# Optimization experiments

Hardware: AMD Instinct MI355X
Metric: run time of the kernel (lower is better)

Reference implementation:

```python
import jax, jax.numpy as jnp
import numpy as np

D_MODEL = 512
NUM_HEADS = 8
HEAD_DIM = D_MODEL // NUM_HEADS  # 64
B, L = 8, 1024


def setup_inputs() -> dict:
    key = jax.random.key(0)
    ks = jax.random.split(key, 6)
    scale = 1.0 / np.sqrt(D_MODEL)
    return {
        "x": jax.random.normal(ks[0], (B, L, D_MODEL), dtype=jnp.float32),
        "mask": jax.random.normal(ks[1], (L, L), dtype=jnp.float32),
        "Wqkv": jax.random.normal(ks[2], (D_MODEL, 3 * D_MODEL), dtype=jnp.float32) * scale,
        "bqkv": jax.random.normal(ks[3], (3 * D_MODEL,), dtype=jnp.float32) * 0.01,
        "Wo": jax.random.normal(ks[4], (D_MODEL, D_MODEL), dtype=jnp.float32) * scale,
        "bo": jax.random.normal(ks[5], (D_MODEL,), dtype=jnp.float32) * 0.01,
    }


def reference(x, mask, Wqkv, bqkv, Wo, bo):
    b, l, _ = x.shape
    qkv = x @ Wqkv + bqkv                                   # [B, L, 3*D]
    # Faithful to torch: reshape to [B, L, H, 3*head_dim] then chunk last dim.
    qkv = qkv.reshape(b, l, NUM_HEADS, 3 * HEAD_DIM)
    qkv = jnp.transpose(qkv, (0, 2, 1, 3))                  # [B, H, L, 3*hd]
    q, k, v = jnp.split(qkv, 3, axis=-1)                    # each [B, H, L, hd]
    scaled = jnp.einsum("bhqd,bhkd->bhqk", q, k) / np.sqrt(HEAD_DIM)
    scaled = scaled + mask                                  # mask broadcasts over [B, H]
    attn = jax.nn.softmax(scaled, axis=-1)
    out = jnp.einsum("bhqk,bhkd->bhqd", attn, v)            # [B, H, L, hd]
    out = jnp.transpose(out, (0, 2, 1, 3)).reshape(b, l, D_MODEL)
    return out @ Wo + bo
```

## Files before the change

kernel.cpp:

```cpp
#include <hip/hip_runtime.h>
#include <hip/hip_bf16.h>
#include <stdint.h>

#define B_ 8
#define L_ 1024
#define DM 512
#define H_ 8
#define HD 64
#define N3 1536
#define M_T (B_*L_)
#define LOG2E 1.44269504f

typedef __attribute__((ext_vector_type(8))) short short8;
typedef __attribute__((ext_vector_type(4))) float f32x4;
typedef __attribute__((ext_vector_type(4))) float float4_t;
typedef __attribute__((ext_vector_type(4))) unsigned short ushort4_t;
typedef __attribute__((ext_vector_type(2))) unsigned int u32x2;

#define MFMA16(a,b,c) __builtin_amdgcn_mfma_f32_16x16x32_bf16((a),(b),(c),0,0,0)

__device__ __forceinline__ short f2bf(float f){
  union { float f; unsigned u; } v; v.f = f;
  unsigned r = v.u + 0x7fffu + ((v.u >> 16) & 1u);
  return (short)(r >> 16);
}

__device__ __forceinline__ short f2bf_fast(float f){
  __hip_bfloat16 h = __float2bfloat16(f);
  short s; __builtin_memcpy(&s, &h, 2); return s;
}

__global__ __launch_bounds__(256) void k_cvt(const float* __restrict__ x,
                                             short* __restrict__ xb, int n8){
  int i = blockIdx.x*256 + threadIdx.x;
  if (i >= n8) return;
  const float4_t* p = (const float4_t*)x + (size_t)i*2;
  float4_t a = p[0], b = p[1];
  short8 o;
  o[0]=f2bf(a[0]); o[1]=f2bf(a[1]); o[2]=f2bf(a[2]); o[3]=f2bf(a[3]);
  o[4]=f2bf(b[0]); o[5]=f2bf(b[1]); o[6]=f2bf(b[2]); o[7]=f2bf(b[3]);
  *((short8*)xb + i) = o;
}

__global__ __launch_bounds__(256) void k_tr2(const float* __restrict__ W0, short* __restrict__ WT0,
                                             const float* __restrict__ W1, short* __restrict__ WT1){
  __shared__ float t[64][65];
  const float* W; short* WT; int N, n0;
  if (blockIdx.x < 24){ W = W0; WT = WT0; N = N3; n0 = blockIdx.x*64; }
  else                { W = W1; WT = WT1; N = DM; n0 = (blockIdx.x-24)*64; }
  int k0 = blockIdx.y*64;
  int tid = threadIdx.x;
  int r = tid >> 4, c4 = (tid & 15) * 4;
  #pragma unroll
  for (int it=0; it<4; ++it){
    int rr = r + it*16;
    float4_t v = *(const float4_t*)(W + (size_t)(k0+rr)*N + n0 + c4);
    t[rr][c4+0]=v[0]; t[rr][c4+1]=v[1]; t[rr][c4+2]=v[2]; t[rr][c4+3]=v[3];
  }
  __syncthreads();
  #pragma unroll
  for (int it=0; it<4; ++it){
    int n = r + it*16;
    ushort4_t o;
    o[0]=(unsigned short)f2bf(t[c4+0][n]);
    o[1]=(unsigned short)f2bf(t[c4+1][n]);
    o[2]=(unsigned short)f2bf(t[c4+2][n]);
    o[3]=(unsigned short)f2bf(t[c4+3][n]);
    *(ushort4_t*)(WT + (size_t)(n0+n)*DM + k0 + c4) = o;
  }
}

__global__ __launch_bounds__(256) void k_maskp(const float* __restrict__ mask,
                                               float* __restrict__ maskP){
  int gid = blockIdx.x*256 + threadIdx.x;
  int nf  = gid & 3;
  int lane= (gid>>2) & 63;
  int kvt = (gid>>8) & 15;
  int qg  = gid>>12;
  int li = lane & 15, lg = lane >> 4;
  int row = qg*16 + li;
  int col = kvt*64 + nf*16 + lg*4;
  float4_t m = *(const float4_t*)(mask + (size_t)row*1024 + col);
  float4_t o;
  #pragma unroll
  for (int j=0;j<4;++j) o[j] = fmaf(m[j], LOG2E, -17.3123405f);
  ((float4_t*)maskP)[gid] = o;
}

__global__ __launch_bounds__(256) void k_gemm_qkv(
    const short* __restrict__ A, const short* __restrict__ Bt,
    const float* __restrict__ bias,
    short* __restrict__ Qo, short* __restrict__ Ko, short* __restrict__ VTo)
{
  __shared__ __align__(16) short As[2][128*40];
  __shared__ __align__(16) short Bs[2][128*40];
  const int m0 = blockIdx.x*128, n0 = blockIdx.y*128;
  const int tid = threadIdx.x;
  const int w = tid>>6, lane = tid&63, li = lane&15, lg = lane>>4;
  const int wr = (w>>1)*64, wc = (w&1)*64;

  int row[2], seg[2];
  #pragma unroll
  for (int c=0;c<2;++c){ int s = tid + c*256; row[c]=s>>2; seg[c]=s&3; }

  short8 ga[2], gb[2];
  #pragma unroll
  for (int c=0;c<2;++c){
    ga[c] = *(const short8*)(A  + (size_t)(m0+row[c])*DM + seg[c]*8);
    gb[c] = *(const short8*)(Bt + (size_t)(n0+row[c])*DM + seg[c]*8);
  }

  const f32x4 fz = {0.f,0.f,0.f,0.f};
  f32x4 acc[4][4];
  #pragma unroll
  for (int i=0;i<4;++i)
    #pragma unroll
    for (int j=0;j<4;++j) acc[i][j] = fz;

  for (int kt=0; kt<16; ++kt){
    short* as = As[kt&1]; short* bs = Bs[kt&1];
    #pragma unroll
    for (int c=0;c<2;++c){
      *(short8*)&as[row[c]*40 + seg[c]*8] = ga[c];
      *(short8*)&bs[row[c]*40 + seg[c]*8] = gb[c];
    }
    __syncthreads();
    if (kt < 15){
      int k0 = (kt+1)*32;
      #pragma unroll
      for (int c=0;c<2;++c){
        ga[c] = *(const short8*)(A  + (size_t)(m0+row[c])*DM + k0 + seg[c]*8);
        gb[c] = *(const short8*)(Bt + (size_t)(n0+row[c])*DM + k0 + seg[c]*8);
      }
    }
    short8 bfr[4];
    #pragma unroll
    for (int nf=0;nf<4;++nf)
      bfr[nf] = *(const short8*)&bs[(wc + nf*16 + li)*40 + lg*8];
    __builtin_amdgcn_s_setprio(1);
    #pragma unroll
    for (int mf=0;mf<4;++mf){
      short8 af = *(const short8*)&as[(wr + mf*16 + li)*40 + lg*8];
      #pragma unroll
      for (int nf=0;nf<4;++nf)
        acc[mf][nf] = MFMA16(af, bfr[nf], acc[mf][nf]);
    }
    __builtin_amdgcn_s_setprio(0);
    __syncthreads();
  }

  #pragma unroll
  for (int nf=0;nf<4;++nf){
    int n = n0 + wc + nf*16 + li;
    float bv = bias[n];
    unsigned h  = (unsigned)n / 192u;
    unsigned wn = (unsigned)n % 192u;
    unsigned typ = wn >> 6, d = wn & 63u;
    #pragma unroll
    for (int mf=0;mf<4;++mf){
      #pragma unroll
      for (int j=0;j<4;++j){
        int m  = m0 + wr + mf*16 + lg*4 + j;
        int b  = m >> 10, lp = m & 1023;
        size_t bh = (size_t)(b*8 + (int)h);
        float vf = acc[mf][nf][j] + bv;
        if (typ == 0)      Qo [(bh<<16) + ((size_t)lp<<6)  + d]  = f2bf_fast(vf * 0.18033688f);
        else if (typ == 1) Ko [(bh<<16) + ((size_t)lp<<6)  + d]  = f2bf_fast(vf);
        else               VTo[(bh<<16) + ((size_t)d<<10)  + lp] = f2bf_fast(vf);
      }
    }
  }
}

__global__ __launch_bounds__(256, 2) void k_attn(
    const short* __restrict__ Q, const short* __restrict__ Kb,
    const short* __restrict__ VT, const float* __restrict__ maskP,
    short* __restrict__ O2)
{
  __shared__ __align__(16) short Ks[2][64*72];
  __shared__ __align__(16) short Vs[2][64*72];
  __shared__ __align__(16) short Ps[4][32*72];
  const int bh = blockIdx.y;
  const int q0 = blockIdx.x*128;
  const int tid = threadIdx.x, w = tid>>6, lane = tid&63, li = lane&15, lg = lane>>4;
  const int qw = q0 + w*32;

  const short* Qp = Q  + ((size_t)bh<<16);
  const short* Kp = Kb + ((size_t)bh<<16);
  const short* Vp = VT + ((size_t)bh<<16);

  short8 qf[2][2];
  #pragma unroll
  for (int mb=0;mb<2;++mb)
    #pragma unroll
    for (int t=0;t<2;++t)
      qf[mb][t] = *(const short8*)(Qp + ((size_t)(qw+mb*16+li)<<6) + t*32 + lg*8);

  short8 ones8;
  #pragma unroll
  for (int e=0;e<8;++e) ones8[e] = (short)0x3f80;

  const f32x4 fz = {0.f,0.f,0.f,0.f};
  f32x4 o[2][4], osum[2];
  #pragma unroll
  for (int mb=0;mb<2;++mb){
    osum[mb] = fz;
    #pragma unroll
    for (int df=0;df<4;++df) o[mb][df] = fz;
  }

  int srow[2], sseg[2];
  #pragma unroll
  for (int c=0;c<2;++c){ int f = tid + c*256; srow[c]=f>>3; sseg[c]=(f&7)*8; }

  short8 gk[2], gv[2];
  #pragma unroll
  for (int c=0;c<2;++c){
    gk[c] = *(const short8*)(Kp + ((size_t)srow[c]<<6)  + sseg[c]);
    gv[c] = *(const short8*)(Vp + ((size_t)srow[c]<<10) + sseg[c]);
  }
  #pragma unroll
  for (int c=0;c<2;++c){
    *(short8*)&Ks[0][srow[c]*72 + sseg[c]] = gk[c];
    *(short8*)&Vs[0][srow[c]*72 + sseg[c]] = gv[c];
  }
  #pragma unroll
  for (int c=0;c<2;++c){
    gk[c] = *(const short8*)(Kp + ((size_t)(64+srow[c])<<6) + sseg[c]);
    gv[c] = *(const short8*)(Vp + ((size_t)srow[c]<<10) + 64 + sseg[c]);
  }

  const float* mpb[2];
  #pragma unroll
  for (int mb=0;mb<2;++mb)
    mpb[mb] = maskP + ((size_t)((qw>>4)+mb)<<14) + lane*16;
  f32x4 mnx[2][4];
  #pragma unroll
  for (int mb=0;mb<2;++mb)
    #pragma unroll
    for (int nf=0;nf<4;++nf)
      mnx[mb][nf] = *(const float4_t*)(mpb[mb] + nf*4);

  __syncthreads();

  short* pw = Ps[w];

  for (int kvt=0; kvt<16; ++kvt){
    const short* ks = Ks[kvt&1];
    const short* vs = Vs[kvt&1];
    if (kvt < 15){
      short* kd = Ks[(kvt&1)^1]; short* vd = Vs[(kvt&1)^1];
      #pragma unroll
      for (int c=0;c<2;++c){
        *(short8*)&kd[srow[c]*72 + sseg[c]] = gk[c];
        *(short8*)&vd[srow[c]*72 + sseg[c]] = gv[c];
      }
    }
    if (kvt < 14){
      int nx = (kvt+2)*64;
      #pragma unroll
      for (int c=0;c<2;++c){
        gk[c] = *(const short8*)(Kp + ((size_t)(nx+srow[c])<<6) + sseg[c]);
        gv[c] = *(const short8*)(Vp + ((size_t)srow[c]<<10) + nx + sseg[c]);
      }
    }

    f32x4 s[2][4];
    __builtin_amdgcn_s_setprio(1);
    #pragma unroll
    for (int nf=0;nf<4;++nf){
      short8 kf0 = *(const short8*)&ks[(nf*16+li)*72 + lg*8];
      short8 kf1 = *(const short8*)&ks[(nf*16+li)*72 + 32 + lg*8];
      #pragma unroll
      for (int mb=0;mb<2;++mb){
        s[mb][nf] = MFMA16(kf0, qf[mb][0], mnx[mb][nf]);
        s[mb][nf] = MFMA16(kf1, qf[mb][1], s[mb][nf]);
      }
    }
    __builtin_amdgcn_s_setprio(0);

    if (kvt < 15){
      #pragma unroll
      for (int mb=0;mb<2;++mb)
        #pragma unroll
        for (int nf=0;nf<4;++nf)
          mnx[mb][nf] = *(const float4_t*)(mpb[mb] + (kvt+1)*1024 + nf*4);
    }

    #pragma unroll
    for (int mb=0;mb<2;++mb){
      #pragma unroll
      for (int nf=0;nf<4;++nf){
        float e0 = exp2f(s[mb][nf][0]), e1 = exp2f(s[mb][nf][1]);
        float e2 = exp2f(s[mb][nf][2]), e3 = exp2f(s[mb][nf][3]);
        unsigned p01, p23;
        asm("v_cvt_pk_bf16_f32 %0, %1, %2" : "=v"(p01) : "v"(e0), "v"(e1));
        asm("v_cvt_pk_bf16_f32 %0, %1, %2" : "=v"(p23) : "v"(e2), "v"(e3));
        u32x2 pv; pv[0]=p01; pv[1]=p23;
        *(u32x2*)&pw[(mb*16+li)*72 + nf*16 + lg*4] = pv;
      }
    }

    __builtin_amdgcn_s_setprio(1);
    #pragma unroll
    for (int t=0;t<2;++t){
      short8 pf0 = *(const short8*)&pw[(   li)*72 + t*32 + lg*8];
      short8 pf1 = *(const short8*)&pw[(16+li)*72 + t*32 + lg*8];
      osum[0] = MFMA16(pf0, ones8, osum[0]);
      osum[1] = MFMA16(pf1, ones8, osum[1]);
      #pragma unroll
      for (int df=0;df<4;++df){
        short8 vf = *(const short8*)&vs[(df*16+li)*72 + t*32 + lg*8];
        o[0][df] = MFMA16(pf0, vf, o[0][df]);
        o[1][df] = MFMA16(pf1, vf, o[1][df]);
      }
    }
    __builtin_amdgcn_s_setprio(0);

    __syncthreads();
  }

  int b = bh >> 3, h = bh & 7;
  #pragma unroll
  for (int mb=0;mb<2;++mb){
    float rl[4];
    #pragma unroll
    for (int j=0;j<4;++j) rl[j] = 1.0f / osum[mb][j];
    #pragma unroll
    for (int df=0;df<4;++df)
      #pragma unroll
      for (int j=0;j<4;++j){
        int m   = b*1024 + qw + mb*16 + lg*4 + j;
        int col = h*64 + df*16 + li;
        O2[(size_t)m*512 + col] = f2bf_fast(o[mb][df][j] * rl[j]);
      }
  }
}

__global__ __launch_bounds__(256) void k_gemm_out(
    const short* __restrict__ A, const short* __restrict__ Bt,
    const float* __restrict__ bias, float* __restrict__ out)
{
  __shared__ __align__(16) short As[2][128*40];
  __shared__ __align__(16) short Bs[2][128*40];
  const int m0 = blockIdx.x*128, n0 = blockIdx.y*128;
  const int tid = threadIdx.x;
  const int w = tid>>6, lane = tid&63, li = lane&15, lg = lane>>4;
  const int wr = (w>>1)*64, wc = (w&1)*64;

  int row[2], seg[2];
  #pragma unroll
  for (int c=0;c<2;++c){ int s = tid + c*256; row[c]=s>>2; seg[c]=s&3; }

  short8 ga[2], gb[2];
  #pragma unroll
  for (int c=0;c<2;++c){
    ga[c] = *(const short8*)(A  + (size_t)(m0+row[c])*DM + seg[c]*8);
    gb[c] = *(const short8*)(Bt + (size_t)(n0+row[c])*DM + seg[c]*8);
  }

  const f32x4 fz = {0.f,0.f,0.f,0.f};
  f32x4 acc[4][4];
  #pragma unroll
  for (int i=0;i<4;++i)
    #pragma unroll
    for (int j=0;j<4;++j) acc[i][j] = fz;

  for (int kt=0; kt<16; ++kt){
    short* as = As[kt&1]; short* bs = Bs[kt&1];
    #pragma unroll
    for (int c=0;c<2;++c){
      *(short8*)&as[row[c]*40 + seg[c]*8] = ga[c];
      *(short8*)&bs[row[c]*40 + seg[c]*8] = gb[c];
    }
    __syncthreads();
    if (kt < 15){
      int k0 = (kt+1)*32;
      #pragma unroll
      for (int c=0;c<2;++c){
        ga[c] = *(const short8*)(A  + (size_t)(m0+row[c])*DM + k0 + seg[c]*8);
        gb[c] = *(const short8*)(Bt + (size_t)(n0+row[c])*DM + k0 + seg[c]*8);
      }
    }
    short8 bfr[4];
    #pragma unroll
    for (int nf=0;nf<4;++nf)
      bfr[nf] = *(const short8*)&bs[(wc + nf*16 + li)*40 + lg*8];
    __builtin_amdgcn_s_setprio(1);
    #pragma unroll
    for (int mf=0;mf<4;++mf){
      short8 af = *(const short8*)&as[(wr + mf*16 + li)*40 + lg*8];
      #pragma unroll
      for (int nf=0;nf<4;++nf)
        acc[mf][nf] = MFMA16(af, bfr[nf], acc[mf][nf]);
    }
    __builtin_amdgcn_s_setprio(0);
    __syncthreads();
  }

  #pragma unroll
  for (int nf=0;nf<4;++nf){
    int n = n0 + wc + nf*16 + li;
    float bv = bias[n];
    #pragma unroll
    for (int mf=0;mf<4;++mf){
      #pragma unroll
      for (int j=0;j<4;++j){
        int m = m0 + wr + mf*16 + lg*4 + j;
        out[(size_t)m*DM + n] = acc[mf][nf][j] + bv;
      }
    }
  }
}

extern "C" void kernel_launch(void* const* d_in, const int* in_sizes, int n_in,
                              void* d_out, int out_size, void* d_ws, size_t ws_size,
                              hipStream_t stream)
{
  (void)in_sizes; (void)n_in; (void)out_size; (void)ws_size;
  const float* x    = (const float*)d_in[0];
  const float* mask = (const float*)d_in[1];
  const float* Wqkv = (const float*)d_in[2];
  const float* bqkv = (const float*)d_in[3];
  const float* Wo   = (const float*)d_in[4];
  const float* bo   = (const float*)d_in[5];
  float* out = (float*)d_out;

  short* xb    = (short*)d_ws;
  short* WqkvT = xb    + (size_t)M_T*DM;
  short* WoT   = WqkvT + (size_t)N3*DM;
  short* Qb    = WoT   + (size_t)DM*DM;
  short* Kbf   = Qb    + (size_t)64*1024*64;
  short* VTb   = Kbf   + (size_t)64*1024*64;
  short* O2    = VTb   + (size_t)64*1024*64;
  float* maskP = (float*)xb;

  k_cvt<<<2048, 256, 0, stream>>>(x, xb, (M_T*DM)/8);
  k_tr2<<<dim3(32, 8), 256, 0, stream>>>(Wqkv, WqkvT, Wo, WoT);
  k_gemm_qkv<<<dim3(M_T/128, N3/128), 256, 0, stream>>>(xb, WqkvT, bqkv, Qb, Kbf, VTb);
  k_maskp<<<1024, 256, 0, stream>>>(mask, maskP);
  k_attn    <<<dim3(L_/128, B_*H_),   256, 0, stream>>>(Qb, Kbf, VTb, maskP, O2);
  k_gemm_out<<<dim3(M_T/128, DM/128), 256, 0, stream>>>(O2, WoT, bo, out);
}
```

Before: 89.86 us.

## Stage GEMM and attention tiles via direct global-to-LDS loads with XOR swizzle

Replaces register-staged global loads and LDS stores in both GEMMs and the attention kernel with global_load_lds direct transfers into unpadded LDS tiles. The attention K/V tiles use an XOR swizzle to avoid bank conflicts, and the attention grid is flattened and remapped so neighbouring blocks cover different heads. exp2f is also swapped for the hardware exp2 builtin. This frees registers and VALU work spent on staging, but the GEMM tiles lose their padding, which may cause LDS bank conflicts, and correctness depends on the async load waits around the barriers.

```diff
diff --git a/kernel.cpp b/kernel.cpp
--- a/kernel.cpp
+++ b/kernel.cpp
@@ -18,6 +18,10 @@
 typedef __attribute__((ext_vector_type(2))) unsigned int u32x2;
 
 #define MFMA16(a,b,c) __builtin_amdgcn_mfma_f32_16x16x32_bf16((a),(b),(c),0,0,0)
+
+#define GLL(gp, lp) __builtin_amdgcn_global_load_lds( \
+    (const __attribute__((address_space(1))) void*)(gp), \
+    (__attribute__((address_space(3))) void*)(lp), 16, 0, 0)
 
 __device__ __forceinline__ short f2bf(float f){
   union { float f; unsigned u; } v; v.f = f;
@@ -92,23 +96,21 @@
     const float* __restrict__ bias,
     short* __restrict__ Qo, short* __restrict__ Ko, short* __restrict__ VTo)
 {
-  __shared__ __align__(16) short As[2][128*40];
-  __shared__ __align__(16) short Bs[2][128*40];
+  __shared__ __align__(16) short As[2][128*32];
+  __shared__ __align__(16) short Bs[2][128*32];
   const int m0 = blockIdx.x*128, n0 = blockIdx.y*128;
   const int tid = threadIdx.x;
   const int w = tid>>6, lane = tid&63, li = lane&15, lg = lane>>4;
   const int wr = (w>>1)*64, wc = (w&1)*64;
 
-  int row[2], seg[2];
-  #pragma unroll
-  for (int c=0;c<2;++c){ int s = tid + c*256; row[c]=s>>2; seg[c]=s&3; }
-
-  short8 ga[2], gb[2];
-  #pragma unroll
-  for (int c=0;c<2;++c){
-    ga[c] = *(const short8*)(A  + (size_t)(m0+row[c])*DM + seg[c]*8);
-    gb[c] = *(const short8*)(Bt + (size_t)(n0+row[c])*DM + seg[c]*8);
-  }
+  const int srow0 = tid>>2, sslot0 = tid&3;
+
+  #define G1_STAGE(buf, kt) do { \
+    GLL(A  + (size_t)(m0+srow0   )*DM + (kt)*32 + sslot0*8, &As[buf][tid*8]); \
+    GLL(A  + (size_t)(m0+srow0+64)*DM + (kt)*32 + sslot0*8, &As[buf][(tid+256)*8]); \
+    GLL(Bt + (size_t)(n0+srow0   )*DM + (kt)*32 + sslot0*8, &Bs[buf][tid*8]); \
+    GLL(Bt + (size_t)(n0+srow0+64)*DM + (kt)*32 + sslot0*8, &Bs[buf][(tid+256)*8]); \
+  } while(0)
 
   const f32x4 fz = {0.f,0.f,0.f,0.f};
   f32x4 acc[4][4];
@@ -117,30 +119,20 @@
     #pragma unroll
     for (int j=0;j<4;++j) acc[i][j] = fz;
 
+  G1_STAGE(0, 0);
+  __syncthreads();
+
   for (int kt=0; kt<16; ++kt){
-    short* as = As[kt&1]; short* bs = Bs[kt&1];
-    #pragma unroll
-    for (int c=0;c<2;++c){
-      *(short8*)&as[row[c]*40 + seg[c]*8] = ga[c];
-      *(short8*)&bs[row[c]*40 + seg[c]*8] = gb[c];
-    }
-    __syncthreads();
-    if (kt < 15){
-      int k0 = (kt+1)*32;
-      #pragma unroll
-      for (int c=0;c<2;++c){
-        ga[c] = *(const short8*)(A  + (size_t)(m0+row[c])*DM + k0 + seg[c]*8);
-        gb[c] = *(const short8*)(Bt + (size_t)(n0+row[c])*DM + k0 + seg[c]*8);
-      }
-    }
+    const short* as = As[kt&1]; const short* bs = Bs[kt&1];
+    if (kt < 15) G1_STAGE((kt&1)^1, kt+1);
     short8 bfr[4];
     #pragma unroll
     for (int nf=0;nf<4;++nf)
-      bfr[nf] = *(const short8*)&bs[(wc + nf*16 + li)*40 + lg*8];
+      bfr[nf] = *(const short8*)&bs[(wc + nf*16 + li)*32 + lg*8];
     __builtin_amdgcn_s_setprio(1);
     #pragma unroll
     for (int mf=0;mf<4;++mf){
-      short8 af = *(const short8*)&as[(wr + mf*16 + li)*40 + lg*8];
+      short8 af = *(const short8*)&as[(wr + mf*16 + li)*32 + lg*8];
       #pragma unroll
       for (int nf=0;nf<4;++nf)
         acc[mf][nf] = MFMA16(af, bfr[nf], acc[mf][nf]);
@@ -170,6 +162,7 @@
       }
     }
   }
+  #undef G1_STAGE
 }
 
 __global__ __launch_bounds__(256, 2) void k_attn(
@@ -177,11 +170,14 @@
     const short* __restrict__ VT, const float* __restrict__ maskP,
     short* __restrict__ O2)
 {
-  __shared__ __align__(16) short Ks[2][64*72];
-  __shared__ __align__(16) short Vs[2][64*72];
+  __shared__ __align__(16) short Ks[2][64*64];
+  __shared__ __align__(16) short Vs[2][64*64];
   __shared__ __align__(16) short Ps[4][32*72];
-  const int bh = blockIdx.y;
-  const int q0 = blockIdx.x*128;
+
+  const int id  = blockIdx.x;
+  const int bh  = (id & 7)*8 + ((id >> 3) & 7);
+  const int q0  = (id >> 6) * 128;
+
   const int tid = threadIdx.x, w = tid>>6, lane = tid&63, li = lane&15, lg = lane>>4;
   const int qw = q0 + w*32;
 
@@ -189,6 +185,16 @@
   const short* Kp = Kb + ((size_t)bh<<16);
   const short* Vp = VT + ((size_t)bh<<16);
 
+  const int arow0 = tid>>3;
+  const int ags0  = (tid&7) ^ (arow0&7);
+
+  #define ATTN_STAGE(buf, nx) do { \
+    GLL(Kp + ((size_t)((nx)+arow0   )<<6) + ags0*8, &Ks[buf][tid*8]); \
+    GLL(Kp + ((size_t)((nx)+arow0+32)<<6) + ags0*8, &Ks[buf][(tid+256)*8]); \
+    GLL(Vp + ((size_t)(arow0   )<<10) + (nx) + ags0*8, &Vs[buf][tid*8]); \
+    GLL(Vp + ((size_t)(arow0+32)<<10) + (nx) + ags0*8, &Vs[buf][(tid+256)*8]); \
+  } while(0)
+
   short8 qf[2][2];
   #pragma unroll
   for (int mb=0;mb<2;++mb)
@@ -207,27 +213,6 @@
     osum[mb] = fz;
     #pragma unroll
     for (int df=0;df<4;++df) o[mb][df] = fz;
-  }
-
-  int srow[2], sseg[2];
-  #pragma unroll
-  for (int c=0;c<2;++c){ int f = tid + c*256; srow[c]=f>>3; sseg[c]=(f&7)*8; }
-
-  short8 gk[2], gv[2];
-  #pragma unroll
-  for (int c=0;c<2;++c){
-    gk[c] = *(const short8*)(Kp + ((size_t)srow[c]<<6)  + sseg[c]);
-    gv[c] = *(const short8*)(Vp + ((size_t)srow[c]<<10) + sseg[c]);
-  }
-  #pragma unroll
-  for (int c=0;c<2;++c){
-    *(short8*)&Ks[0][srow[c]*72 + sseg[c]] = gk[c];
-    *(short8*)&Vs[0][srow[c]*72 + sseg[c]] = gv[c];
-  }
-  #pragma unroll
-  for (int c=0;c<2;++c){
-    gk[c] = *(const short8*)(Kp + ((size_t)(64+srow[c])<<6) + sseg[c]);
-    gv[c] = *(const short8*)(Vp + ((size_t)srow[c]<<10) + 64 + sseg[c]);
   }
 
   const float* mpb[2];
@@ -241,36 +226,23 @@
     for (int nf=0;nf<4;++nf)
       mnx[mb][nf] = *(const float4_t*)(mpb[mb] + nf*4);
 
+  ATTN_STAGE(0, 0);
   __syncthreads();
 
   short* pw = Ps[w];
+  const int sw = li & 7;
 
   for (int kvt=0; kvt<16; ++kvt){
     const short* ks = Ks[kvt&1];
     const short* vs = Vs[kvt&1];
-    if (kvt < 15){
-      short* kd = Ks[(kvt&1)^1]; short* vd = Vs[(kvt&1)^1];
-      #pragma unroll
-      for (int c=0;c<2;++c){
-        *(short8*)&kd[srow[c]*72 + sseg[c]] = gk[c];
-        *(short8*)&vd[srow[c]*72 + sseg[c]] = gv[c];
-      }
-    }
-    if (kvt < 14){
-      int nx = (kvt+2)*64;
-      #pragma unroll
-      for (int c=0;c<2;++c){
-        gk[c] = *(const short8*)(Kp + ((size_t)(nx+srow[c])<<6) + sseg[c]);
-        gv[c] = *(const short8*)(Vp + ((size_t)srow[c]<<10) + nx + sseg[c]);
-      }
-    }
+    if (kvt < 15) ATTN_STAGE((kvt&1)^1, (kvt+1)*64);
 
     f32x4 s[2][4];
     __builtin_amdgcn_s_setprio(1);
     #pragma unroll
     for (int nf=0;nf<4;++nf){
-      short8 kf0 = *(const short8*)&ks[(nf*16+li)*72 + lg*8];
-      short8 kf1 = *(const short8*)&ks[(nf*16+li)*72 + 32 + lg*8];
+      short8 kf0 = *(const short8*)&ks[(nf*16+li)*64 + ((  lg)^sw)*8];
+      short8 kf1 = *(const short8*)&ks[(nf*16+li)*64 + ((4|lg)^sw)*8];
       #pragma unroll
       for (int mb=0;mb<2;++mb){
         s[mb][nf] = MFMA16(kf0, qf[mb][0], mnx[mb][nf]);
@@ -291,8 +263,10 @@
     for (int mb=0;mb<2;++mb){
       #pragma unroll
       for (int nf=0;nf<4;++nf){
-        float e0 = exp2f(s[mb][nf][0]), e1 = exp2f(s[mb][nf][1]);
-        float e2 = exp2f(s[mb][nf][2]), e3 = exp2f(s[mb][nf][3]);
+        float e0 = __builtin_amdgcn_exp2f(s[mb][nf][0]);
+        float e1 = __builtin_amdgcn_exp2f(s[mb][nf][1]);
+        float e2 = __builtin_amdgcn_exp2f(s[mb][nf][2]);
+        float e3 = __builtin_amdgcn_exp2f(s[mb][nf][3]);
         unsigned p01, p23;
         asm("v_cvt_pk_bf16_f32 %0, %1, %2" : "=v"(p01) : "v"(e0), "v"(e1));
         asm("v_cvt_pk_bf16_f32 %0, %1, %2" : "=v"(p23) : "v"(e2), "v"(e3));
@@ -310,7 +284,7 @@
       osum[1] = MFMA16(pf1, ones8, osum[1]);
       #pragma unroll
       for (int df=0;df<4;++df){
-        short8 vf = *(const short8*)&vs[(df*16+li)*72 + t*32 + lg*8];
+        short8 vf = *(const short8*)&vs[(df*16+li)*64 + (((t<<2)|lg)^sw)*8];
         o[0][df] = MFMA16(pf0, vf, o[0][df]);
         o[1][df] = MFMA16(pf1, vf, o[1][df]);
       }
@@ -319,6 +293,7 @@
 
     __syncthreads();
   }
+  #undef ATTN_STAGE
 
   int b = bh >> 3, h = bh & 7;
   #pragma unroll
@@ -341,23 +316,21 @@
     const short* __restrict__ A, const short* __restrict__ Bt,
     const float* __restrict__ bias, float* __restrict__ out)
 {
-  __shared__ __align__(16) short As[2][128*40];
-  __shared__ __align__(16) short Bs[2][128*40];
+  __shared__ __align__(16) short As[2][128*32];
+  __shared__ __align__(16) short Bs[2][128*32];
   const int m0 = blockIdx.x*128, n0 = blockIdx.y*128;
   const int tid = threadIdx.x;
   const int w = tid>>6, lane = tid&63, li = lane&15, lg = lane>>4;
   const int wr = (w>>1)*64, wc = (w&1)*64;
 
-  int row[2], seg[2];
-  #pragma unroll
-  for (int c=0;c<2;++c){ int s = tid + c*256; row[c]=s>>2; seg[c]=s&3; }
-
-  short8 ga[2], gb[2];
-  #pragma unroll
-  for (int c=0;c<2;++c){
-    ga[c] = *(const short8*)(A  + (size_t)(m0+row[c])*DM + seg[c]*8);
-    gb[c] = *(const short8*)(Bt + (size_t)(n0+row[c])*DM + seg[c]*8);
-  }
+  const int srow0 = tid>>2, sslot0 = tid&3;
+
+  #define G2_STAGE(buf, kt) do { \
+    GLL(A  + (size_t)(m0+srow0   )*DM + (kt)*32 + sslot0*8, &As[buf][tid*8]); \
+    GLL(A  + (size_t)(m0+srow0+64)*DM + (kt)*32 + sslot0*8, &As[buf][(tid+256)*8]); \
+    GLL(Bt + (size_t)(n0+srow0   )*DM + (kt)*32 + sslot0*8, &Bs[buf][tid*8]); \
+    GLL(Bt + (size_t)(n0+srow0+64)*DM + (kt)*32 + sslot0*8, &Bs[buf][(tid+256)*8]); \
+  } while(0)
 
   const f32x4 fz = {0.f,0.f,0.f,0.f};
   f32x4 acc[4][4];
@@ -366,30 +339,20 @@
     #pragma unroll
     for (int j=0;j<4;++j) acc[i][j] = fz;
 
+  G2_STAGE(0, 0);
+  __syncthreads();
+
   for (int kt=0; kt<16; ++kt){
-    short* as = As[kt&1]; short* bs = Bs[kt&1];
-    #pragma unroll
-    for (int c=0;c<2;++c){
-      *(short8*)&as[row[c]*40 + seg[c]*8] = ga[c];
-      *(short8*)&bs[row[c]*40 + seg[c]*8] = gb[c];
-    }
-    __syncthreads();
-    if (kt < 15){
-      int k0 = (kt+1)*32;
-      #pragma unroll
-      for (int c=0;c<2;++c){
-        ga[c] = *(const short8*)(A  + (size_t)(m0+row[c])*DM + k0 + seg[c]*8);
-        gb[c] = *(const short8*)(Bt + (size_t)(n0+row[c])*DM + k0 + seg[c]*8);
-      }
-    }
+    const short* as = As[kt&1]; const short* bs = Bs[kt&1];
+    if (kt < 15) G2_STAGE((kt&1)^1, kt+1);
     short8 bfr[4];
     #pragma unroll
     for (int nf=0;nf<4;++nf)
-      bfr[nf] = *(const short8*)&bs[(wc + nf*16 + li)*40 + lg*8];
+      bfr[nf] = *(const short8*)&bs[(wc + nf*16 + li)*32 + lg*8];
     __builtin_amdgcn_s_setprio(1);
     #pragma unroll
     for (int mf=0;mf<4;++mf){
-      short8 af = *(const short8*)&as[(wr + mf*16 + li)*40 + lg*8];
+      short8 af = *(const short8*)&as[(wr + mf*16 + li)*32 + lg*8];
       #pragma unroll
       for (int nf=0;nf<4;++nf)
         acc[mf][nf] = MFMA16(af, bfr[nf], acc[mf][nf]);
@@ -411,6 +374,7 @@
       }
     }
   }
+  #undef G2_STAGE
 }
 
 extern "C" void kernel_launch(void* const* d_in, const int* in_sizes, int n_in,
@@ -439,6 +403,6 @@
   k_tr2<<<dim3(32, 8), 256, 0, stream>>>(Wqkv, WqkvT, Wo, WoT);
   k_gemm_qkv<<<dim3(M_T/128, N3/128), 256, 0, stream>>>(xb, WqkvT, bqkv, Qb, Kbf, VTb);
   k_maskp<<<1024, 256, 0, stream>>>(mask, maskP);
-  k_attn    <<<dim3(L_/128, B_*H_),   256, 0, stream>>>(Qb, Kbf, VTb, maskP, O2);
+  k_attn    <<<512, 256, 0, stream>>>(Qb, Kbf, VTb, maskP, O2);
   k_gemm_out<<<dim3(M_T/128, DM/128), 256, 0, stream>>>(O2, WoT, bo, out);
 }
```

After: 84.44 us. 6.0% less time.
